# Optimization experiments

Hardware: AMD Instinct MI355X
Metric: run time of the kernel (lower is better)

Reference implementation:

```python
import jax, jax.numpy as jnp
import numpy as np


def _rel_pos_log(ws):
    coords = np.stack(np.meshgrid(np.arange(ws), np.arange(ws), indexing='ij'))  # [2,ws,ws]
    cf = coords.reshape(2, -1)
    rel = (cf[:, :, None] - cf[:, None, :]).transpose(1, 2, 0).astype(np.float32)  # [N,N,2]
    return np.sign(rel) * np.log1p(np.abs(rel))


def _conv1x1(x, w, b):
    return jnp.einsum('bchw,oc->bohw', x, w) + b[None, :, None, None]


def _conv3x3_reflect(x, w, b):
    xp = jnp.pad(x, ((0, 0), (0, 0), (1, 1), (1, 1)), mode='reflect')
    y = jax.lax.conv_general_dilated(xp, w, (1, 1), 'VALID',
                                     dimension_numbers=('NCHW', 'OIHW', 'NCHW'))
    return y + b[None, :, None, None]


def setup_inputs() -> dict:
    key = jax.random.key(0)
    ks = jax.random.split(key, 8)
    dim, nh = 96, 6
    s = 0.02
    return {
        'X': jax.random.normal(ks[0], (4, dim, 256, 256), jnp.float32),
        'V_w': jax.random.normal(ks[1], (dim, dim), jnp.float32) * s,
        'V_b': jnp.zeros((dim,), jnp.float32),
        'QK_w': jax.random.normal(ks[2], (2 * dim, dim), jnp.float32) * s,
        'QK_b': jnp.zeros((2 * dim,), jnp.float32),
        'meta_w1': jax.random.normal(ks[3], (2, 256), jnp.float32) * 0.1,
        'meta_b1': jnp.zeros((256,), jnp.float32),
        'meta_w2': jax.random.normal(ks[4], (256, nh), jnp.float32) * 0.1,
        'meta_b2': jnp.zeros((nh,), jnp.float32),
        'conv1_w': jax.random.normal(ks[5], (dim, dim, 3, 3), jnp.float32) * s,
        'conv1_b': jnp.zeros((dim,), jnp.float32),
        'conv2_w': jax.random.normal(ks[6], (dim, dim, 3, 3), jnp.float32) * s,
        'conv2_b': jnp.zeros((dim,), jnp.float32),
        'proj_w': jax.random.normal(ks[7], (dim, dim), jnp.float32) * s,
        'proj_b': jnp.zeros((dim,), jnp.float32),
        'window_size': 8,
        'num_heads': 6,
    }


def reference(X, V_w, V_b, QK_w, QK_b, meta_w1, meta_b1, meta_w2, meta_b2,
              conv1_w, conv1_b, conv2_w, conv2_b, proj_w, proj_b,
              window_size, num_heads):
    B, C, H, W = X.shape
    ws = int(window_size)
    nh = int(num_heads)
    hd = C // nh
    scale = hd ** (-0.5)

    V = _conv1x1(X, V_w, V_b)                     # [B,C,H,W]
    QK = _conv1x1(X, QK_w, QK_b)                  # [B,2C,H,W]
    QKV = jnp.concatenate([QK, V], axis=1)        # [B,3C,H,W]

    # window partition (shift_size=0, H,W divisible by ws -> no padding)
    x = QKV.transpose(0, 2, 3, 1)                 # [B,H,W,3C]
    x = x.reshape(B, H // ws, ws, W // ws, ws, 3 * C)
    x = x.transpose(0, 1, 3, 2, 4, 5).reshape(-1, ws * ws, 3 * C)  # [nW,N,3C]

    qkv = x.reshape(-1, ws * ws, 3, nh, hd).transpose(2, 0, 3, 1, 4)
    q, k, v = qkv[0] * scale, qkv[1], qkv[2]      # [nW,nh,N,hd]
    attn = jnp.einsum('bhnd,bhmd->bhnm', q, k)    # [nW,nh,N,N]

    rp = jnp.asarray(_rel_pos_log(ws))            # [N,N,2]
    bias = jax.nn.relu(rp @ meta_w1 + meta_b1) @ meta_w2 + meta_b2  # [N,N,nh]
    attn = attn + bias.transpose(2, 0, 1)[None]
    attn = jax.nn.softmax(attn, axis=-1)

    o = jnp.einsum('bhnm,bhmd->bhnd', attn, v)    # [nW,nh,N,hd]
    o = o.transpose(0, 2, 1, 3).reshape(-1, ws * ws, C)

    # window reverse
    o = o.reshape(B, H // ws, W // ws, ws, ws, C)
    o = o.transpose(0, 1, 3, 2, 4, 5).reshape(B, H, W, C)
    attn_out = o.transpose(0, 3, 1, 2)            # [B,C,H,W]

    conv_out = _conv3x3_reflect(jax.nn.relu(_conv3x3_reflect(V, conv1_w, conv1_b)),
                                conv2_w, conv2_b)
    out = _conv1x1(conv_out + attn_out, proj_w, proj_b)
    return out
```

## Files before the change

### kernel.cpp

```cpp
#include <hip/hip_runtime.h>
#include <cmath>

typedef short  short8 __attribute__((ext_vector_type(8)));
typedef float  f32x4  __attribute__((ext_vector_type(4)));
typedef unsigned short us8 __attribute__((ext_vector_type(8)));
typedef unsigned short us4 __attribute__((ext_vector_type(4)));

constexpr int kHW = 65536;
constexpr int kP  = 262144;

__device__ __forceinline__ unsigned short f2bf(float x) {
  unsigned u = __builtin_bit_cast(unsigned, x);
  u += 0x7fffu + ((u >> 16) & 1u);
  return (unsigned short)(u >> 16);
}
__device__ __forceinline__ float bf2f(unsigned short h) {
  unsigned u = ((unsigned)h) << 16;
  return __builtin_bit_cast(float, u);
}
__device__ __forceinline__ void split2(float v, unsigned short& h, unsigned short& l) {
  unsigned short hh = f2bf(v);
  h = hh;
  l = f2bf(v - bf2f(hh));
}
__device__ __forceinline__ void gload16(const void* g, void* l) {
  __builtin_amdgcn_global_load_lds(
      (const __attribute__((address_space(1))) void*)g,
      (__attribute__((address_space(3))) void*)l, 16, 0, 0);
}
#define CFENCE() asm volatile("" ::: "memory")
#define WAITVM7() asm volatile("s_waitcnt vmcnt(7)" ::: "memory")
#define WAITVM0() asm volatile("s_waitcnt vmcnt(0)" ::: "memory")
#define SBAR() __builtin_amdgcn_s_barrier()

__global__ void bias_kernel(const float* __restrict__ w1, const float* __restrict__ b1,
                            const float* __restrict__ w2, const float* __restrict__ b2,
                            float* __restrict__ bias_tab) {
  int i = blockIdx.x;
  int j = threadIdx.x;
  float dy = (float)((i >> 3) - (j >> 3));
  float dx = (float)((i & 7) - (j & 7));
  float r0 = copysignf(log1pf(fabsf(dy)), dy);
  float r1 = copysignf(log1pf(fabsf(dx)), dx);
  float acc[6];
#pragma unroll
  for (int h = 0; h < 6; ++h) acc[h] = b2[h];
  for (int t = 0; t < 256; ++t) {
    float hv = fmaf(r0, w1[t], fmaf(r1, w1[256 + t], b1[t]));
    hv = fmaxf(hv, 0.f);
#pragma unroll
    for (int h = 0; h < 6; ++h) acc[h] = fmaf(hv, w2[t * 6 + h], acc[h]);
  }
#pragma unroll
  for (int h = 0; h < 6; ++h) bias_tab[h * 4096 + i * 64 + j] = acc[h];
}

__global__ void prep_weights(const float* __restrict__ qk_w, const float* __restrict__ v_w,
                             const float* __restrict__ c1w, const float* __restrict__ c2w,
                             const float* __restrict__ pjw,
                             unsigned short* __restrict__ Wqh, unsigned short* __restrict__ Wql,
                             unsigned short* __restrict__ W1h,
                             unsigned short* __restrict__ W2h,
                             unsigned short* __restrict__ Wph, unsigned short* __restrict__ Wpl) {
  int i = blockIdx.x * 256 + threadIdx.x;
  if (i < 27648) {
    float v = (i < 18432) ? qk_w[i] : v_w[i - 18432];
    split2(v, Wqh[i], Wql[i]);
  }
  if (i < 82944) {
    int dlt = i / 9216;
    int oc  = (i / 96) % 96;
    int ic  = i % 96;
    int src = (oc * 96 + ic) * 9 + dlt;
    W1h[i] = f2bf(c1w[src]);
    W2h[i] = f2bf(c2w[src]);
  }
  if (i < 9216) split2(pjw[i], Wph[i], Wpl[i]);
}

__global__ __launch_bounds__(256) void split_x(const float* __restrict__ X,
                                               unsigned short* __restrict__ Xh) {
  __shared__ float tile[96][65];
  int t = threadIdx.x;
  size_t p0 = (size_t)blockIdx.x * 64;
  int b = (int)(p0 >> 16), pix = (int)(p0 & 65535);
  const float* xb = X + (size_t)b * 96 * kHW + pix;
#pragma unroll
  for (int i = 0; i < 24; ++i) {
    int ic = (t >> 6) + i * 4;
    tile[ic][t & 63] = xb[(size_t)ic * kHW + (t & 63)];
  }
  __syncthreads();
  int px = t >> 2;
  size_t outbase = (p0 + px) * 96;
#pragma unroll
  for (int cc = 0; cc < 3; ++cc) {
    int c = (t & 3) + cc * 4;
    us8 h8;
#pragma unroll
    for (int j = 0; j < 8; ++j) h8[j] = f2bf(tile[c * 8 + j][px]);
    *(us8*)(Xh + outbase + c * 8) = h8;
  }
}

__global__ __launch_bounds__(256, 2) void qkv_gemm(
    const unsigned short* __restrict__ Wqh, const unsigned short* __restrict__ Wql,
    const unsigned short* __restrict__ Xh,
    const float* __restrict__ qk_b, const float* __restrict__ v_b,
    unsigned short* __restrict__ Qp, unsigned short* __restrict__ Kp,
    unsigned short* __restrict__ Vp) {
  int t = threadIdx.x, wv = t >> 6, lane = t & 63;
  size_t px0 = (size_t)blockIdx.x * 256 + wv * 64;
  int col = lane & 15, g = lane >> 4;

  const char* bH = (const char*)Xh + ((px0 + col) * 96 + g * 8) * 2;
  short8 Bh[3][4];
#pragma unroll
  for (int ks = 0; ks < 3; ++ks)
#pragma unroll
    for (int nf = 0; nf < 4; ++nf)
      Bh[ks][nf] = *(const short8*)(bH + (size_t)(nf * 16 * 96 + ks * 32) * 2);

#pragma unroll 1
  for (int z = 0; z < 3; ++z) {
    f32x4 acc[6][4];
#pragma unroll
    for (int m = 0; m < 6; ++m)
#pragma unroll
      for (int n = 0; n < 4; ++n) acc[m][n] = (f32x4)0.f;
    const char* aH = (const char*)(Wqh + z * 9216) + (size_t)(col * 96 + g * 8) * 2;
    const char* aL = (const char*)(Wql + z * 9216) + (size_t)(col * 96 + g * 8) * 2;
#pragma unroll
    for (int ks = 0; ks < 3; ++ks) {
      short8 Ah[6], Al[6];
#pragma unroll
      for (int mf = 0; mf < 6; ++mf) {
        Ah[mf] = *(const short8*)(aH + (size_t)(mf * 16 * 96 + ks * 32) * 2);
        Al[mf] = *(const short8*)(aL + (size_t)(mf * 16 * 96 + ks * 32) * 2);
      }
#pragma unroll
      for (int mf = 0; mf < 6; ++mf)
#pragma unroll
        for (int nf = 0; nf < 4; ++nf) {
          acc[mf][nf] = __builtin_amdgcn_mfma_f32_16x16x32_bf16(Ah[mf], Bh[ks][nf], acc[mf][nf], 0, 0, 0);
          acc[mf][nf] = __builtin_amdgcn_mfma_f32_16x16x32_bf16(Al[mf], Bh[ks][nf], acc[mf][nf], 0, 0, 0);
        }
    }
    const float* bias = (z == 0) ? qk_b : (z == 1 ? qk_b + 96 : v_b);
    float scale = (z == 0) ? 0.25f : 1.f;
    unsigned short* dst = (z == 0) ? Qp : (z == 1 ? Kp : Vp);
#pragma unroll
    for (int mf = 0; mf < 6; ++mf) {
      int oc0 = mf * 16 + g * 4;
      f32x4 bv;
#pragma unroll
      for (int r = 0; r < 4; ++r) bv[r] = bias[oc0 + r];
#pragma unroll
      for (int nf = 0; nf < 4; ++nf) {
        size_t p = px0 + nf * 16 + col;
        f32x4 v = (acc[mf][nf] + bv) * scale;
        us4 o;
#pragma unroll
        for (int r = 0; r < 4; ++r) o[r] = f2bf(v[r]);
        *(us4*)(dst + ((size_t)mf * kP + p) * 16 + g * 4) = o;
      }
    }
  }
}

__global__ __launch_bounds__(256) void attn_mfma(
    const unsigned short* __restrict__ Qp, const unsigned short* __restrict__ Kp,
    const unsigned short* __restrict__ Vp, const float* __restrict__ bias_tab,
    unsigned short* __restrict__ out) {
  __shared__ unsigned short PT[4][64 * 72];
  __shared__ unsigned short VT[4][16 * 72];
  __shared__ float rls[4][64];

  int t = threadIdx.x;
  int wv = t >> 6, lane = t & 63;
  int l15 = lane & 15, g = lane >> 4;
  int h = blockIdx.y;
  int wid = blockIdx.x * 4 + wv;
  int b = wid >> 10, wy = (wid >> 5) & 31, wx = wid & 31;
  size_t p0 = ((size_t)b << 16) + (size_t)wy * 8 * 256 + (size_t)wx * 8;
  const float* bt = bias_tab + h * 4096;

  f32x4 acc[4][4];
#pragma unroll
  for (int kf = 0; kf < 4; ++kf)
#pragma unroll
    for (int qf = 0; qf < 4; ++qf)
      acc[kf][qf] = *(const f32x4*)(bt + (qf * 16 + l15) * 64 + kf * 16 + g * 4);

  short8 Af[4], Bf[4];
#pragma unroll
  for (int f = 0; f < 4; ++f) {
    int kk = f * 16 + l15;
    size_t pk = p0 + (size_t)(kk >> 3) * 256 + (kk & 7);
    if (g < 2) {
      Af[f] = *(const short8*)(Kp + ((size_t)h * kP + pk) * 16 + g * 8);
      Bf[f] = *(const short8*)(Qp + ((size_t)h * kP + pk) * 16 + g * 8);
    } else {
      Af[f] = (short8)0;
      Bf[f] = (short8)0;
    }
  }

  {
    size_t pv = p0 + (size_t)(lane >> 3) * 256 + (lane & 7);
    const unsigned short* vp = Vp + ((size_t)h * kP + pv) * 16;
    us8 v0 = *(const us8*)(vp), v1 = *(const us8*)(vp + 8);
    unsigned short* vt = VT[wv];
#pragma unroll
    for (int d = 0; d < 8; ++d) {
      vt[d * 72 + lane]       = v0[d];
      vt[(d + 8) * 72 + lane] = v1[d];
    }
  }

#pragma unroll
  for (int kf = 0; kf < 4; ++kf)
#pragma unroll
    for (int qf = 0; qf < 4; ++qf)
      acc[kf][qf] = __builtin_amdgcn_mfma_f32_16x16x32_bf16(Af[kf], Bf[qf], acc[kf][qf], 0, 0, 0);

#pragma unroll
  for (int qf = 0; qf < 4; ++qf) {
    float m = acc[0][qf][0];
#pragma unroll
    for (int kf = 0; kf < 4; ++kf)
#pragma unroll
      for (int r = 0; r < 4; ++r) m = fmaxf(m, acc[kf][qf][r]);
    m = fmaxf(m, __shfl_xor(m, 16));
    m = fmaxf(m, __shfl_xor(m, 32));
    float sum = 0.f;
#pragma unroll
    for (int kf = 0; kf < 4; ++kf)
#pragma unroll
      for (int r = 0; r < 4; ++r) {
        float pe = __expf(acc[kf][qf][r] - m);
        acc[kf][qf][r] = pe;
        sum += pe;
      }
    sum += __shfl_xor(sum, 16);
    sum += __shfl_xor(sum, 32);
    if (g == 0) rls[wv][qf * 16 + l15] = 1.f / sum;
  }

  unsigned short* pt = PT[wv];
#pragma unroll
  for (int qf = 0; qf < 4; ++qf)
#pragma unroll
    for (int kf = 0; kf < 4; ++kf) {
      us4 pb;
#pragma unroll
      for (int r = 0; r < 4; ++r) pb[r] = f2bf(acc[kf][qf][r]);
      *(us4*)&pt[(qf * 16 + l15) * 72 + kf * 16 + g * 4] = pb;
    }

  short8 Pa[4][2], Vb[2];
#pragma unroll
  for (int qf = 0; qf < 4; ++qf)
#pragma unroll
    for (int kc = 0; kc < 2; ++kc)
      Pa[qf][kc] = *(const short8*)&pt[(qf * 16 + l15) * 72 + kc * 32 + g * 8];
#pragma unroll
  for (int kc = 0; kc < 2; ++kc)
    Vb[kc] = *(const short8*)&VT[wv][l15 * 72 + kc * 32 + g * 8];
  f32x4 o[4];
#pragma unroll
  for (int qf = 0; qf < 4; ++qf) {
    o[qf] = (f32x4)0.f;
#pragma unroll
    for (int kc = 0; kc < 2; ++kc)
      o[qf] = __builtin_amdgcn_mfma_f32_16x16x32_bf16(Pa[qf][kc], Vb[kc], o[qf], 0, 0, 0);
  }

#pragma unroll
  for (int qf = 0; qf < 4; ++qf) {
    f32x4 rv = *(const f32x4*)&rls[wv][qf * 16 + g * 4];
#pragma unroll
    for (int r = 0; r < 4; ++r)
      pt[(qf * 16 + g * 4 + r) * 72 + l15] = f2bf(o[qf][r] * rv[r]);
  }
  {
    int q = lane;
    us8 o0 = *(const us8*)&pt[q * 72];
    us8 o1 = *(const us8*)&pt[q * 72 + 8];
    size_t pq = p0 + (size_t)(q >> 3) * 256 + (q & 7);
    unsigned short* op = out + ((size_t)h * kP + pq) * 16;
    *(us8*)(op)     = o0;
    *(us8*)(op + 8) = o1;
  }
}

constexpr int kSlotB = 26624;

__device__ __forceinline__ void stage_rows(const char* __restrict__ rowbase,
                                           char* slot, const int (&off)[7], int t) {
  int wvbase = t & 192;
#pragma unroll
  for (int i = 0; i < 6; ++i)
    gload16(rowbase + off[i], slot + (i * 256 + wvbase) * 16);
  gload16(rowbase + off[6], slot + 1536 * 16);
}

__device__ __forceinline__ void conv_dy(
    const char* __restrict__ lds, const unsigned short* __restrict__ Wh,
    int tap0, int och, int xq, int col, int g, f32x4 (&acc)[3][4]) {
#pragma unroll
  for (int dx = 0; dx < 3; ++dx) {
    const char* ah = (const char*)Wh + ((size_t)(tap0 + dx) * 9216 + och * 4608 + col * 96 + g * 8) * 2;
    int ppb = xq * 64 + col + dx;
#pragma unroll
    for (int ks = 0; ks < 3; ++ks) {
      short8 Ah[3], Bf[4];
#pragma unroll
      for (int mf = 0; mf < 3; ++mf)
        Ah[mf] = *(const short8*)(ah + (size_t)(mf * 16 * 96 + ks * 32) * 2);
#pragma unroll
      for (int nf = 0; nf < 4; ++nf) {
        int pp = ppb + nf * 16;
        Bf[nf] = *(const short8*)(lds + ks * 8320 + ((g ^ (pp & 3)) * 2080) + pp * 16);
      }
#pragma unroll
      for (int mf = 0; mf < 3; ++mf)
#pragma unroll
        for (int nf = 0; nf < 4; ++nf)
          acc[mf][nf] = __builtin_amdgcn_mfma_f32_16x16x32_bf16(Ah[mf], Bf[nf], acc[mf][nf], 0, 0, 0);
    }
  }
}

template <int MODE>
__global__ __launch_bounds__(256, 3) void conv_gl(
    const unsigned short* __restrict__ Wh,
    const unsigned short* __restrict__ B_, const float* __restrict__ bias,
    const unsigned short* __restrict__ attn, unsigned short* __restrict__ O_) {
  __shared__ char lds[2][kSlotB];
  int t = threadIdx.x, wv = t >> 6, lane = t & 63;
  int col = lane & 15, g = lane >> 4;
  int och = wv >> 1, xq = wv & 1;
  int bid = blockIdx.x;
  int g8 = (bid & 7) * 256 + (bid >> 3);
  int xh = g8 & 1;
  int ry = g8 >> 1;
  int b = ry >> 8, y = ry & 255;
  int x0 = xh * 128;

  int off[7];
#pragma unroll
  for (int i = 0; i < 7; ++i) {
    int idx = (i < 6) ? (i * 256 + t) : (1536 + (t & 63));
    if (idx > 1559) idx = 1559;
    int ks = idx / 520;
    int rem = idx - ks * 520;
    int gp = rem / 130;
    int pp = rem - gp * 130;
    int c8 = ks * 4 + (gp ^ (pp & 3));
    int xx = x0 - 1 + pp;
    xx = xx < 0 ? 1 : (xx > 255 ? 254 : xx);
    if (MODE == 0)
      off[i] = (((c8 >> 1) * kP + xx) * 16 + (c8 & 1) * 8) * 2;
    else
      off[i] = (xx * 96 + c8 * 8) * 2;
  }

  const size_t rowBytes = (MODE == 0) ? (size_t)256 * 32 : (size_t)256 * 192;
  const char* Bbase = (const char*)B_ + (size_t)b * kHW * ((MODE == 0) ? 32 : 192);
  int ym = (y == 0) ? 1 : y - 1;
  int yp = (y == 255) ? 254 : y + 1;

  f32x4 acc[3][4];
#pragma unroll
  for (int m = 0; m < 3; ++m)
#pragma unroll
    for (int n = 0; n < 4; ++n) acc[m][n] = (f32x4)0.f;

  stage_rows(Bbase + (size_t)ym * rowBytes, lds[0], off, t);
  CFENCE();
  stage_rows(Bbase + (size_t)y  * rowBytes, lds[1], off, t);
  WAITVM7(); SBAR();
  conv_dy(lds[0], Wh, 0, och, xq, col, g, acc);
  SBAR();
  stage_rows(Bbase + (size_t)yp * rowBytes, lds[0], off, t);
  WAITVM7(); SBAR();
  conv_dy(lds[1], Wh, 3, och, xq, col, g, acc);
  WAITVM0(); SBAR();
  conv_dy(lds[0], Wh, 6, och, xq, col, g, acc);

  char* tb = lds[1];
  size_t prow = (size_t)b * kHW + (size_t)y * 256;
#pragma unroll
  for (int mf = 0; mf < 3; ++mf) {
    int oc0 = och * 48 + mf * 16 + g * 4;
    f32x4 bv;
#pragma unroll
    for (int r = 0; r < 4; ++r) bv[r] = bias[oc0 + r];
#pragma unroll
    for (int nf = 0; nf < 4; ++nf) {
      int pp = xq * 64 + nf * 16 + col;
      f32x4 v = acc[mf][nf] + bv;
      if (MODE == 0) {
#pragma unroll
        for (int r = 0; r < 4; ++r) v[r] = fmaxf(v[r], 0.f);
      } else {
        size_t p = prow + x0 + pp;
        us4 a4 = *(const us4*)(attn + ((size_t)(och * 3 + mf) * kP + p) * 16 + g * 4);
#pragma unroll
        for (int r = 0; r < 4; ++r) v[r] += bf2f(a4[r]);
      }
      us4 o;
#pragma unroll
      for (int r = 0; r < 4; ++r) o[r] = f2bf(v[r]);
      *(us4*)(tb + pp * 208 + oc0 * 2) = o;
    }
  }
  __syncthreads();
  {
    int pp = t >> 1, half = t & 1;
    const char* src = tb + pp * 208 + half * 96;
    us8 o0 = *(const us8*)(src);
    us8 o1 = *(const us8*)(src + 16);
    us8 o2 = *(const us8*)(src + 32);
    us8 o3 = *(const us8*)(src + 48);
    us8 o4 = *(const us8*)(src + 64);
    us8 o5 = *(const us8*)(src + 80);
    unsigned short* dst = O_ + (prow + x0) * 96 + (size_t)t * 48;
    *(us8*)(dst)      = o0;
    *(us8*)(dst + 8)  = o1;
    *(us8*)(dst + 16) = o2;
    *(us8*)(dst + 24) = o3;
    *(us8*)(dst + 32) = o4;
    *(us8*)(dst + 40) = o5;
  }
}

__global__ __launch_bounds__(256, 2) void proj_gemm(
    const unsigned short* __restrict__ Wph, const unsigned short* __restrict__ Wpl,
    const unsigned short* __restrict__ S_, const float* __restrict__ bias,
    float* __restrict__ out) {
  int t = threadIdx.x, wv = t >> 6, lane = t & 63;
  size_t px0 = (size_t)blockIdx.x * 256 + wv * 64;
  int col = lane & 15, g = lane >> 4;
  f32x4 acc[6][4];
#pragma unroll
  for (int m = 0; m < 6; ++m)
#pragma unroll
    for (int n = 0; n < 4; ++n) acc[m][n] = (f32x4)0.f;
  const char* aH = (const char*)Wph + (size_t)(col * 96 + g * 8) * 2;
  const char* aL = (const char*)Wpl + (size_t)(col * 96 + g * 8) * 2;
  const char* bH = (const char*)S_ + ((px0 + col) * 96 + g * 8) * 2;
#pragma unroll
  for (int ks = 0; ks < 3; ++ks) {
    short8 Ah[6], Al[6], Bf[4];
#pragma unroll
    for (int mf = 0; mf < 6; ++mf) {
      Ah[mf] = *(const short8*)(aH + (size_t)(mf * 16 * 96 + ks * 32) * 2);
      Al[mf] = *(const short8*)(aL + (size_t)(mf * 16 * 96 + ks * 32) * 2);
    }
#pragma unroll
    for (int nf = 0; nf < 4; ++nf)
      Bf[nf] = *(const short8*)(bH + (size_t)(nf * 16 * 96 + ks * 32) * 2);
#pragma unroll
    for (int mf = 0; mf < 6; ++mf)
#pragma unroll
      for (int nf = 0; nf < 4; ++nf) {
        acc[mf][nf] = __builtin_amdgcn_mfma_f32_16x16x32_bf16(Ah[mf], Bf[nf], acc[mf][nf], 0, 0, 0);
        acc[mf][nf] = __builtin_amdgcn_mfma_f32_16x16x32_bf16(Al[mf], Bf[nf], acc[mf][nf], 0, 0, 0);
      }
  }
#pragma unroll
  for (int mf = 0; mf < 6; ++mf) {
    int oc0 = mf * 16 + g * 4;
#pragma unroll
    for (int nf = 0; nf < 4; ++nf) {
      size_t p = px0 + nf * 16 + col;
      size_t bb = p >> 16, pix = p & 65535;
      f32x4 v = acc[mf][nf];
#pragma unroll
      for (int r = 0; r < 4; ++r)
        out[(bb * 96 + oc0 + r) * (size_t)kHW + pix] = v[r] + bias[oc0 + r];
    }
  }
}

extern "C" void kernel_launch(void* const* d_in, const int* in_sizes, int n_in,
                              void* d_out, int out_size, void* d_ws, size_t ws_size,
                              hipStream_t stream) {
  const float* X       = (const float*)d_in[0];
  const float* V_w     = (const float*)d_in[1];
  const float* V_b     = (const float*)d_in[2];
  const float* QK_w    = (const float*)d_in[3];
  const float* QK_b    = (const float*)d_in[4];
  const float* meta_w1 = (const float*)d_in[5];
  const float* meta_b1 = (const float*)d_in[6];
  const float* meta_w2 = (const float*)d_in[7];
  const float* meta_b2 = (const float*)d_in[8];
  const float* conv1_w = (const float*)d_in[9];
  const float* conv1_b = (const float*)d_in[10];
  const float* conv2_w = (const float*)d_in[11];
  const float* conv2_b = (const float*)d_in[12];
  const float* proj_w  = (const float*)d_in[13];
  const float* proj_b  = (const float*)d_in[14];
  float* out = (float*)d_out;

  char* w = (char*)d_ws;
  const size_t PLANE = (size_t)kP * 96 * 2;
  unsigned short* Xh = (unsigned short*)(w + 0 * PLANE);
  unsigned short* Qp = (unsigned short*)(w + 1 * PLANE);
  unsigned short* Kp = (unsigned short*)(w + 2 * PLANE);
  unsigned short* Vp = (unsigned short*)(w + 3 * PLANE);
  float* bias_tab    = (float*)(w + 4 * PLANE);
  unsigned short* Wqh = (unsigned short*)(w + 4 * PLANE + 98304);
  unsigned short* Wql = Wqh + 27648;
  unsigned short* W1h = Wql + 27648;
  unsigned short* W2h = W1h + 82944;
  unsigned short* Wph = W2h + 82944;
  unsigned short* Wpl = Wph + 9216;
  unsigned short* T1r = Xh;
  unsigned short* S2r = Qp;
  unsigned short* attnB = (unsigned short*)out;

  bias_kernel<<<dim3(64), dim3(64), 0, stream>>>(meta_w1, meta_b1, meta_w2, meta_b2, bias_tab);
  prep_weights<<<dim3(324), dim3(256), 0, stream>>>(QK_w, V_w, conv1_w, conv2_w, proj_w,
                                                    Wqh, Wql, W1h, W2h, Wph, Wpl);
  split_x<<<dim3(4096), dim3(256), 0, stream>>>(X, Xh);
  qkv_gemm<<<dim3(1024), dim3(256), 0, stream>>>(Wqh, Wql, Xh, QK_b, V_b, Qp, Kp, Vp);
  attn_mfma<<<dim3(1024, 6), dim3(256), 0, stream>>>(Qp, Kp, Vp, bias_tab, attnB);
  conv_gl<0><<<dim3(2048), dim3(256), 0, stream>>>(W1h, Vp, conv1_b, nullptr, T1r);
  conv_gl<1><<<dim3(2048), dim3(256), 0, stream>>>(W2h, T1r, conv2_b, attnB, S2r);
  proj_gemm<<<dim3(1024), dim3(256), 0, stream>>>(Wph, Wpl, S2r, proj_b, out);
}
```

Baseline: 356.8 us.

## Retile 3x3 conv blocks to two output rows by 64 columns with row reuse

The 3x3 conv kernel now computes two adjacent output rows over a 64-pixel strip per block instead of one row over 128 pixels. It stages four input rows into four LDS slots up front, and each staged row feeds both output rows' accumulators. This cuts the redundant input-row loads from three per output row to two, and shrinks LDS per slot. In exchange it loads weights twice for the shared middle rows, issues all input loads before any compute, which reduces overlap, and doubles the epilogue passes.

```diff
diff --git a/kernel.cpp b/kernel.cpp
--- a/kernel.cpp
+++ b/kernel.cpp
@@ -29,7 +29,7 @@
       (__attribute__((address_space(3))) void*)l, 16, 0, 0);
 }
 #define CFENCE() asm volatile("" ::: "memory")
-#define WAITVM7() asm volatile("s_waitcnt vmcnt(7)" ::: "memory")
+#define WAITVM3() asm volatile("s_waitcnt vmcnt(3)" ::: "memory")
 #define WAITVM0() asm volatile("s_waitcnt vmcnt(0)" ::: "memory")
 #define SBAR() __builtin_amdgcn_s_barrier()
 
@@ -294,41 +294,104 @@
   }
 }
 
-constexpr int kSlotB = 26624;
-
-__device__ __forceinline__ void stage_rows(const char* __restrict__ rowbase,
-                                           char* slot, const int (&off)[7], int t) {
+constexpr int kSlotB = 13312;
+
+__device__ __forceinline__ void stage_row(const char* __restrict__ rowbase,
+                                          char* slot, const int (&off)[4], int t) {
   int wvbase = t & 192;
 #pragma unroll
-  for (int i = 0; i < 6; ++i)
+  for (int i = 0; i < 3; ++i)
     gload16(rowbase + off[i], slot + (i * 256 + wvbase) * 16);
-  gload16(rowbase + off[6], slot + 1536 * 16);
-}
-
-__device__ __forceinline__ void conv_dy(
-    const char* __restrict__ lds, const unsigned short* __restrict__ Wh,
-    int tap0, int och, int xq, int col, int g, f32x4 (&acc)[3][4]) {
+  if (t < 64)
+    gload16(rowbase + off[3], slot + 768 * 16);
+}
+
+template <bool R0, bool R1>
+__device__ __forceinline__ void conv_slot(
+    const char* __restrict__ lds_s, const unsigned short* __restrict__ Wh,
+    int tapY, int tapY1, int och, int xq, int col, int g,
+    f32x4 (&aY)[3][2], f32x4 (&aY1)[3][2]) {
 #pragma unroll
   for (int dx = 0; dx < 3; ++dx) {
-    const char* ah = (const char*)Wh + ((size_t)(tap0 + dx) * 9216 + och * 4608 + col * 96 + g * 8) * 2;
-    int ppb = xq * 64 + col + dx;
+    int ppb = xq * 32 + col + dx;
 #pragma unroll
     for (int ks = 0; ks < 3; ++ks) {
-      short8 Ah[3], Bf[4];
-#pragma unroll
-      for (int mf = 0; mf < 3; ++mf)
-        Ah[mf] = *(const short8*)(ah + (size_t)(mf * 16 * 96 + ks * 32) * 2);
-#pragma unroll
-      for (int nf = 0; nf < 4; ++nf) {
+      short8 Bf[2];
+#pragma unroll
+      for (int nf = 0; nf < 2; ++nf) {
         int pp = ppb + nf * 16;
-        Bf[nf] = *(const short8*)(lds + ks * 8320 + ((g ^ (pp & 3)) * 2080) + pp * 16);
-      }
-#pragma unroll
-      for (int mf = 0; mf < 3; ++mf)
-#pragma unroll
-        for (int nf = 0; nf < 4; ++nf)
-          acc[mf][nf] = __builtin_amdgcn_mfma_f32_16x16x32_bf16(Ah[mf], Bf[nf], acc[mf][nf], 0, 0, 0);
-    }
+        Bf[nf] = *(const short8*)(lds_s + ks * 4224 + ((g ^ (pp & 3)) * 1056) + pp * 16);
+      }
+      if (R0) {
+        const char* ah = (const char*)Wh + ((size_t)(tapY + dx) * 9216 + och * 4608 + col * 96 + g * 8) * 2;
+        short8 Ah[3];
+#pragma unroll
+        for (int mf = 0; mf < 3; ++mf)
+          Ah[mf] = *(const short8*)(ah + (size_t)(mf * 16 * 96 + ks * 32) * 2);
+#pragma unroll
+        for (int mf = 0; mf < 3; ++mf)
+#pragma unroll
+          for (int nf = 0; nf < 2; ++nf)
+            aY[mf][nf] = __builtin_amdgcn_mfma_f32_16x16x32_bf16(Ah[mf], Bf[nf], aY[mf][nf], 0, 0, 0);
+      }
+      if (R1) {
+        const char* ah = (const char*)Wh + ((size_t)(tapY1 + dx) * 9216 + och * 4608 + col * 96 + g * 8) * 2;
+        short8 Ah[3];
+#pragma unroll
+        for (int mf = 0; mf < 3; ++mf)
+          Ah[mf] = *(const short8*)(ah + (size_t)(mf * 16 * 96 + ks * 32) * 2);
+#pragma unroll
+        for (int mf = 0; mf < 3; ++mf)
+#pragma unroll
+          for (int nf = 0; nf < 2; ++nf)
+            aY1[mf][nf] = __builtin_amdgcn_mfma_f32_16x16x32_bf16(Ah[mf], Bf[nf], aY1[mf][nf], 0, 0, 0);
+      }
+    }
+  }
+}
+
+template <int MODE>
+__device__ __forceinline__ void conv_epilogue(
+    f32x4 (&acc)[3][2], char* tb, const float* __restrict__ bias,
+    const unsigned short* __restrict__ attn, unsigned short* __restrict__ O_,
+    int y, int b, int x0, int och, int xq, int col, int g, int t) {
+  size_t prow = (size_t)b * kHW + (size_t)y * 256;
+#pragma unroll
+  for (int mf = 0; mf < 3; ++mf) {
+    int oc0 = och * 48 + mf * 16 + g * 4;
+    f32x4 bv;
+#pragma unroll
+    for (int r = 0; r < 4; ++r) bv[r] = bias[oc0 + r];
+#pragma unroll
+    for (int nf = 0; nf < 2; ++nf) {
+      int pp = xq * 32 + nf * 16 + col;
+      f32x4 v = acc[mf][nf] + bv;
+      if (MODE == 0) {
+#pragma unroll
+        for (int r = 0; r < 4; ++r) v[r] = fmaxf(v[r], 0.f);
+      } else {
+        size_t p = prow + x0 + pp;
+        us4 a4 = *(const us4*)(attn + ((size_t)(och * 3 + mf) * kP + p) * 16 + g * 4);
+#pragma unroll
+        for (int r = 0; r < 4; ++r) v[r] += bf2f(a4[r]);
+      }
+      us4 o;
+#pragma unroll
+      for (int r = 0; r < 4; ++r) o[r] = f2bf(v[r]);
+      *(us4*)(tb + pp * 208 + oc0 * 2) = o;
+    }
+  }
+  __syncthreads();
+  {
+    int px = t >> 2, q = t & 3;
+    const char* src = tb + px * 208 + q * 48;
+    us8 o0 = *(const us8*)(src);
+    us8 o1 = *(const us8*)(src + 16);
+    us8 o2 = *(const us8*)(src + 32);
+    unsigned short* dst = O_ + (prow + x0 + px) * 96 + q * 24;
+    *(us8*)(dst)      = o0;
+    *(us8*)(dst + 8)  = o1;
+    *(us8*)(dst + 16) = o2;
   }
 }
 
@@ -337,26 +400,26 @@
     const unsigned short* __restrict__ Wh,
     const unsigned short* __restrict__ B_, const float* __restrict__ bias,
     const unsigned short* __restrict__ attn, unsigned short* __restrict__ O_) {
-  __shared__ char lds[2][kSlotB];
+  __shared__ char lds[4][kSlotB];
   int t = threadIdx.x, wv = t >> 6, lane = t & 63;
   int col = lane & 15, g = lane >> 4;
   int och = wv >> 1, xq = wv & 1;
   int bid = blockIdx.x;
   int g8 = (bid & 7) * 256 + (bid >> 3);
-  int xh = g8 & 1;
-  int ry = g8 >> 1;
-  int b = ry >> 8, y = ry & 255;
-  int x0 = xh * 128;
-
-  int off[7];
-#pragma unroll
-  for (int i = 0; i < 7; ++i) {
-    int idx = (i < 6) ? (i * 256 + t) : (1536 + (t & 63));
-    if (idx > 1559) idx = 1559;
-    int ks = idx / 520;
-    int rem = idx - ks * 520;
-    int gp = rem / 130;
-    int pp = rem - gp * 130;
+  int xh = g8 & 3;
+  int rp = g8 >> 2;
+  int b = rp >> 7, y0 = (rp & 127) * 2;
+  int x0 = xh * 64;
+
+  int off[4];
+#pragma unroll
+  for (int i = 0; i < 4; ++i) {
+    int idx = (i < 3) ? (i * 256 + t) : (768 + t);
+    if (idx > 791) idx = 791;
+    int ks = idx / 264;
+    int rem = idx - ks * 264;
+    int gp = rem / 66;
+    int pp = rem - gp * 66;
     int c8 = ks * 4 + (gp ^ (pp & 3));
     int xx = x0 - 1 + pp;
     xx = xx < 0 ? 1 : (xx > 255 ? 254 : xx);
@@ -368,72 +431,30 @@
 
   const size_t rowBytes = (MODE == 0) ? (size_t)256 * 32 : (size_t)256 * 192;
   const char* Bbase = (const char*)B_ + (size_t)b * kHW * ((MODE == 0) ? 32 : 192);
-  int ym = (y == 0) ? 1 : y - 1;
-  int yp = (y == 255) ? 254 : y + 1;
-
-  f32x4 acc[3][4];
+  int rA = (y0 == 0) ? 1 : y0 - 1;
+  int rD = (y0 + 2 > 255) ? 254 : y0 + 2;
+
+  f32x4 aY[3][2], aY1[3][2];
 #pragma unroll
   for (int m = 0; m < 3; ++m)
 #pragma unroll
-    for (int n = 0; n < 4; ++n) acc[m][n] = (f32x4)0.f;
-
-  stage_rows(Bbase + (size_t)ym * rowBytes, lds[0], off, t);
-  CFENCE();
-  stage_rows(Bbase + (size_t)y  * rowBytes, lds[1], off, t);
-  WAITVM7(); SBAR();
-  conv_dy(lds[0], Wh, 0, och, xq, col, g, acc);
-  SBAR();
-  stage_rows(Bbase + (size_t)yp * rowBytes, lds[0], off, t);
-  WAITVM7(); SBAR();
-  conv_dy(lds[1], Wh, 3, och, xq, col, g, acc);
+    for (int n = 0; n < 2; ++n) { aY[m][n] = (f32x4)0.f; aY1[m][n] = (f32x4)0.f; }
+
+  stage_row(Bbase + (size_t)rA * rowBytes,       lds[0], off, t); CFENCE();
+  stage_row(Bbase + (size_t)y0 * rowBytes,       lds[1], off, t); CFENCE();
+  stage_row(Bbase + (size_t)(y0 + 1) * rowBytes, lds[2], off, t); CFENCE();
+  stage_row(Bbase + (size_t)rD * rowBytes,       lds[3], off, t);
+  WAITVM3(); SBAR();
+
+  conv_slot<true,  false>(lds[0], Wh, 0, 0, och, xq, col, g, aY, aY1);
+  conv_slot<true,  true >(lds[1], Wh, 3, 0, och, xq, col, g, aY, aY1);
+  conv_slot<true,  true >(lds[2], Wh, 6, 3, och, xq, col, g, aY, aY1);
   WAITVM0(); SBAR();
-  conv_dy(lds[0], Wh, 6, och, xq, col, g, acc);
-
-  char* tb = lds[1];
-  size_t prow = (size_t)b * kHW + (size_t)y * 256;
-#pragma unroll
-  for (int mf = 0; mf < 3; ++mf) {
-    int oc0 = och * 48 + mf * 16 + g * 4;
-    f32x4 bv;
-#pragma unroll
-    for (int r = 0; r < 4; ++r) bv[r] = bias[oc0 + r];
-#pragma unroll
-    for (int nf = 0; nf < 4; ++nf) {
-      int pp = xq * 64 + nf * 16 + col;
-      f32x4 v = acc[mf][nf] + bv;
-      if (MODE == 0) {
-#pragma unroll
-        for (int r = 0; r < 4; ++r) v[r] = fmaxf(v[r], 0.f);
-      } else {
-        size_t p = prow + x0 + pp;
-        us4 a4 = *(const us4*)(attn + ((size_t)(och * 3 + mf) * kP + p) * 16 + g * 4);
-#pragma unroll
-        for (int r = 0; r < 4; ++r) v[r] += bf2f(a4[r]);
-      }
-      us4 o;
-#pragma unroll
-      for (int r = 0; r < 4; ++r) o[r] = f2bf(v[r]);
-      *(us4*)(tb + pp * 208 + oc0 * 2) = o;
-    }
-  }
+  conv_slot<false, true >(lds[3], Wh, 0, 6, och, xq, col, g, aY, aY1);
+
+  conv_epilogue<MODE>(aY,  lds[0], bias, attn, O_, y0,     b, x0, och, xq, col, g, t);
   __syncthreads();
-  {
-    int pp = t >> 1, half = t & 1;
-    const char* src = tb + pp * 208 + half * 96;
-    us8 o0 = *(const us8*)(src);
-    us8 o1 = *(const us8*)(src + 16);
-    us8 o2 = *(const us8*)(src + 32);
-    us8 o3 = *(const us8*)(src + 48);
-    us8 o4 = *(const us8*)(src + 64);
-    us8 o5 = *(const us8*)(src + 80);
-    unsigned short* dst = O_ + (prow + x0) * 96 + (size_t)t * 48;
-    *(us8*)(dst)      = o0;
-    *(us8*)(dst + 8)  = o1;
-    *(us8*)(dst + 16) = o2;
-    *(us8*)(dst + 24) = o3;
-    *(us8*)(dst + 32) = o4;
-    *(us8*)(dst + 40) = o5;
-  }
+  conv_epilogue<MODE>(aY1, lds[0], bias, attn, O_, y0 + 1, b, x0, och, xq, col, g, t);
 }
 
 __global__ __launch_bounds__(256, 2) void proj_gemm(
```

After: 452.4 us. +26.8%, slower.
